# Kernel optimization log

Hardware: AMD Instinct MI355X
Metric: run time of the kernel (lower is better)

Reference implementation:

```python
import jax, jax.numpy as jnp
import numpy as np

L, S, N, E, H = 2048, 2048, 4, 1024, 16
D = E // H


def setup_inputs() -> dict:
    k0 = jax.random.key(0)
    ks = jax.random.split(k0, 11)
    std = 1.0 / np.sqrt(E)
    return {
        "query": jax.random.normal(ks[0], (L, N, E), jnp.float32),
        "key": jax.random.normal(ks[1], (S, N, E), jnp.float32),
        "value": jax.random.normal(ks[2], (S, N, E), jnp.float32),
        "Wq": jax.random.normal(ks[3], (E, E), jnp.float32) * std,
        "bq": jnp.zeros((E,), jnp.float32),
        "Wk": jax.random.normal(ks[4], (E, E), jnp.float32) * std,
        "bk": jnp.zeros((E,), jnp.float32),
        "Wv": jax.random.normal(ks[5], (E, E), jnp.float32) * std,
        "bv": jnp.zeros((E,), jnp.float32),
        "Wo": jax.random.normal(ks[6], (E, E), jnp.float32) * std,
        "bo": jnp.zeros((E,), jnp.float32),
    }


def reference(query, key, value, Wq, bq, Wk, bk, Wv, bv, Wo, bo):
    # projections (torch Linear: x @ W.T + b)
    q = query @ Wq.T + bq  # [L,N,E]
    k = key @ Wk.T + bk    # [S,N,E]
    v = value @ Wv.T + bv  # [S,N,E]
    # split heads -> [N,H,len,D]
    q = q.reshape(L, N, H, D).transpose(1, 2, 0, 3)
    k = k.reshape(S, N, H, D).transpose(1, 2, 0, 3)
    v = v.reshape(S, N, H, D).transpose(1, 2, 0, 3)
    scores = jnp.einsum("nhld,nhsd->nhls", q, k) / np.sqrt(D).astype(np.float32)
    attn_weights = jax.nn.softmax(scores, axis=-1)  # [N,H,L,S]
    out = jnp.einsum("nhls,nhsd->nhld", attn_weights, v)  # [N,H,L,D]
    out = out.transpose(2, 0, 1, 3).reshape(L, N, E)
    attn_output = out @ Wo.T + bo  # [L,N,E]
    # need_weights=True, average_attn_weights=True -> mean over heads
    return attn_output, attn_weights.mean(axis=1)
```

## Files before the change

kernel.cpp:

```cpp
#include <hip/hip_runtime.h>
#include <hip/hip_bf16.h>

typedef __attribute__((ext_vector_type(8))) short short8;
typedef __attribute__((ext_vector_type(4))) float f32x4;

#define AS1 __attribute__((address_space(1)))
#define AS3 __attribute__((address_space(3)))

__device__ __forceinline__ void gload16(const void* g, void* l) {
  __builtin_amdgcn_global_load_lds((const AS1 unsigned int*)g,
                                   (AS3 unsigned int*)l, 16, 0, 0);
}

__device__ __forceinline__ unsigned short f2bf(float x) {
  unsigned u = __float_as_uint(x);
  u = (u + 0x7FFFu + ((u >> 16) & 1u)) >> 16;
  return (unsigned short)u;
}

__device__ __forceinline__ short8 lds8(const unsigned short* p) {
  return *(const short8*)p;
}

__device__ __forceinline__ short8 lds8s(const unsigned short* base, int row, int byteInRow) {
  const int a = (row << 7) + (byteInRow ^ ((row & 7) << 4));
  return *(const short8*)((const char*)base + a);
}

#define LL 2048
#define NB 4
#define EE 1024
#define HH 16
#define DD 64
#define MROWS 8192
#define SC2 0.18033688f
#define MFIX 16.0f

__global__ __launch_bounds__(256) void conv_bf16(const float* __restrict__ src,
                                                 unsigned short* __restrict__ dst) {
  int i = blockIdx.x * 256 + threadIdx.x;
  float4 v = ((const float4*)src)[i];
  ushort4 o;
  o.x = f2bf(v.x); o.y = f2bf(v.y); o.z = f2bf(v.z); o.w = f2bf(v.w);
  ((ushort4*)dst)[i] = o;
}

template <int MODE>
__global__ __launch_bounds__(256) void gemm_bt(const unsigned short* __restrict__ A,
                                               const unsigned short* __restrict__ B,
                                               const float* __restrict__ bias,
                                               unsigned short* __restrict__ outb,
                                               float* __restrict__ outf) {
  constexpr int K = 1024;
  __shared__ __align__(16) unsigned short As[2][64 * 64];
  __shared__ __align__(16) unsigned short Bs[2][64 * 64];
  const int tid = threadIdx.x;
  const int lane = tid & 63, w = tid >> 6;
  const int wr = w >> 1, wc = w & 1;
  const int lrow = lane & 15, lg = lane >> 4;
  const int m0 = blockIdx.y * 128, n0 = blockIdx.x * 128;

  f32x4 acc[4][4] = {};

  const int sr = tid >> 3, sseg = tid & 7;
  const int slog = sseg ^ (sr & 7);
  const int mA = sr + 64 * (slog >> 2);
  const int kof = (slog & 3) * 8;
  const unsigned short* ga  = A + (size_t)(m0 + mA) * K + kof;
  const unsigned short* ga2 = A + (size_t)(m0 + mA + 32) * K + kof;
  const unsigned short* gb  = B + (size_t)(n0 + mA) * K + kof;
  const unsigned short* gb2 = B + (size_t)(n0 + mA + 32) * K + kof;

  gload16(ga,  (char*)As[0] + tid * 16);
  gload16(ga2, (char*)As[0] + tid * 16 + 4096);
  gload16(gb,  (char*)Bs[0] + tid * 16);
  gload16(gb2, (char*)Bs[0] + tid * 16 + 4096);
  __syncthreads();

  int cur = 0;
  for (int k0 = 0; k0 < K; k0 += 32) {
    if (k0 + 32 < K) {
      const int nxt = cur ^ 1;
      gload16(ga  + k0 + 32, (char*)As[nxt] + tid * 16);
      gload16(ga2 + k0 + 32, (char*)As[nxt] + tid * 16 + 4096);
      gload16(gb  + k0 + 32, (char*)Bs[nxt] + tid * 16);
      gload16(gb2 + k0 + 32, (char*)Bs[nxt] + tid * 16 + 4096);
    }

    short8 af[4], bfr[4];
#pragma unroll
    for (int mt = 0; mt < 4; ++mt)
      af[mt] = lds8s(As[cur], mt * 16 + lrow, (wr * 4 + lg) * 16);
#pragma unroll
    for (int nt = 0; nt < 4; ++nt)
      bfr[nt] = lds8s(Bs[cur], nt * 16 + lrow, (wc * 4 + lg) * 16);
#pragma unroll
    for (int mt = 0; mt < 4; ++mt)
#pragma unroll
      for (int nt = 0; nt < 4; ++nt)
        acc[mt][nt] = __builtin_amdgcn_mfma_f32_16x16x32_bf16(af[mt], bfr[nt],
                                                              acc[mt][nt], 0, 0, 0);
    __syncthreads();
    cur ^= 1;
  }

#pragma unroll
  for (int mt = 0; mt < 4; ++mt) {
#pragma unroll
    for (int nt = 0; nt < 4; ++nt) {
      const int col = n0 + wc * 64 + nt * 16 + lrow;
      const float bv = bias[col];
#pragma unroll
      for (int r = 0; r < 4; ++r) {
        const int row = m0 + wr * 64 + mt * 16 + lg * 4 + r;
        const float v = acc[mt][nt][r] + bv;
        if (MODE == 0) {
          const int l = row >> 2, n = row & 3, h = col >> 6, d = col & 63;
          outb[(((size_t)(n * HH + h)) * LL + l) * DD + d] = f2bf(v);
        } else if (MODE == 1) {
          const int s = row >> 2, n = row & 3, h = col >> 6, d = col & 63;
          outb[(((size_t)(n * HH + h)) * DD + d) * LL + s] = f2bf(v);
        } else {
          outf[(size_t)row * EE + col] = v;
        }
      }
    }
  }
}

__global__ __launch_bounds__(256) void flash_attn(const unsigned short* __restrict__ qh,
                                                  const unsigned short* __restrict__ kh,
                                                  const unsigned short* __restrict__ vth,
                                                  unsigned short* __restrict__ oh,
                                                  float* __restrict__ cT) {
  __shared__ __align__(16) unsigned short Ks[64 * 64];
  __shared__ __align__(16) unsigned short Vts[64 * 64];
  __shared__ __align__(16) unsigned short QPs[64 * 64];
  const int tid = threadIdx.x, lane = tid & 63, w = tid >> 6;
  const int lrow = lane & 15, lg = lane >> 4;
  const int nh = blockIdx.y;
  const int l0 = blockIdx.x * 64;

  const unsigned short* qbase = qh + ((size_t)nh * LL + l0) * DD;
  const unsigned short* kbase = kh + (size_t)nh * LL * DD;
  const unsigned short* vbase = vth + (size_t)nh * DD * LL;

  const int sr = tid >> 3;
  const int cs = ((tid & 7) ^ (sr & 7)) * 8;

  gload16(qbase + (size_t)sr * DD + cs,        (char*)QPs + tid * 16);
  gload16(qbase + (size_t)(sr + 32) * DD + cs, (char*)QPs + tid * 16 + 4096);
  gload16(kbase + (size_t)sr * DD + cs,        (char*)Ks + tid * 16);
  gload16(kbase + (size_t)(sr + 32) * DD + cs, (char*)Ks + tid * 16 + 4096);
  gload16(vbase + (size_t)sr * LL + cs,        (char*)Vts + tid * 16);
  gload16(vbase + (size_t)(sr + 32) * LL + cs, (char*)Vts + tid * 16 + 4096);
  __syncthreads();

  short8 qa0 = lds8s(QPs, w * 16 + lrow, lg * 16);
  short8 qa1 = lds8s(QPs, w * 16 + lrow, 64 + lg * 16);

  const short onev = (short)0x3F80;
  const short8 ones = {onev, onev, onev, onev, onev, onev, onev, onev};
  const f32x4 fz = {};

  f32x4 acco[4] = {};
  f32x4 accz = {};

  const unsigned short* kpre = kbase + (size_t)(64 + sr) * DD + cs;
  const unsigned short* vpre = vbase + (size_t)sr * LL + 64 + cs;

  const int prow = w * 16 + lrow;
#pragma unroll 1
  for (int t = 0; t < 32; ++t) {
    const bool pf = (t < 31);

    f32x4 sc[4];
    __builtin_amdgcn_s_setprio(1);
#pragma unroll
    for (int ct = 0; ct < 4; ++ct) {
      short8 b0 = lds8s(Ks, ct * 16 + lrow, lg * 16);
      short8 b1 = lds8s(Ks, ct * 16 + lrow, 64 + lg * 16);
      sc[ct] = __builtin_amdgcn_mfma_f32_16x16x32_bf16(
          b1, qa1,
          __builtin_amdgcn_mfma_f32_16x16x32_bf16(b0, qa0, fz, 0, 0, 0),
          0, 0, 0);
    }
    __builtin_amdgcn_s_setprio(0);

    __syncthreads();
    if (pf) {
      gload16(kpre,                   (char*)Ks + tid * 16);
      gload16(kpre + (size_t)32 * DD, (char*)Ks + tid * 16 + 4096);
      kpre += (size_t)64 * DD;
    }

#pragma unroll
    for (int ct = 0; ct < 4; ++ct) {
      float e0 = __builtin_exp2f(__builtin_fmaf(sc[ct][0], SC2, -MFIX));
      float e1 = __builtin_exp2f(__builtin_fmaf(sc[ct][1], SC2, -MFIX));
      float e2 = __builtin_exp2f(__builtin_fmaf(sc[ct][2], SC2, -MFIX));
      float e3 = __builtin_exp2f(__builtin_fmaf(sc[ct][3], SC2, -MFIX));
      unsigned int p0, p1;
      asm("v_cvt_pk_bf16_f32 %0, %1, %2" : "=v"(p0) : "v"(e0), "v"(e1));
      asm("v_cvt_pk_bf16_f32 %0, %1, %2" : "=v"(p1) : "v"(e2), "v"(e3));
      const int a = (prow << 7) + ((((ct * 2 + (lg >> 1)) ^ (prow & 7)) << 4) | ((lg & 1) << 3));
      uint2 u; u.x = p0; u.y = p1;
      *(uint2*)((char*)QPs + a) = u;
    }

    short8 pa0 = lds8s(QPs, prow, lg * 16);
    short8 pa1 = lds8s(QPs, prow, 64 + lg * 16);
    __builtin_amdgcn_s_setprio(1);
#pragma unroll
    for (int dt = 0; dt < 4; ++dt) {
      short8 vb0 = lds8s(Vts, dt * 16 + lrow, lg * 16);
      short8 vb1 = lds8s(Vts, dt * 16 + lrow, 64 + lg * 16);
      acco[dt] = __builtin_amdgcn_mfma_f32_16x16x32_bf16(vb0, pa0, acco[dt], 0, 0, 0);
      acco[dt] = __builtin_amdgcn_mfma_f32_16x16x32_bf16(vb1, pa1, acco[dt], 0, 0, 0);
    }
    accz = __builtin_amdgcn_mfma_f32_16x16x32_bf16(ones, pa0, accz, 0, 0, 0);
    accz = __builtin_amdgcn_mfma_f32_16x16x32_bf16(ones, pa1, accz, 0, 0, 0);
    __builtin_amdgcn_s_setprio(0);

    __syncthreads();
    if (pf) {
      gload16(vpre,                   (char*)Vts + tid * 16);
      gload16(vpre + (size_t)32 * LL, (char*)Vts + tid * 16 + 4096);
      vpre += 64;
    }
  }

  const int n = nh >> 4, h = nh & 15;
  const int lt = l0 + prow;
  const float zrow = accz[0];
  const float rz = 1.0f / zrow;
#pragma unroll
  for (int dt = 0; dt < 4; ++dt) {
    ushort4 o;
    o.x = f2bf(acco[dt][0] * rz);
    o.y = f2bf(acco[dt][1] * rz);
    o.z = f2bf(acco[dt][2] * rz);
    o.w = f2bf(acco[dt][3] * rz);
    *(ushort4*)&oh[((size_t)lt * NB + n) * EE + h * 64 + dt * 16 + lg * 4] = o;
  }
  if (lg == 0) {
    cT[((size_t)n * LL + lt) * HH + h] = -(MFIX + __builtin_log2f(zrow));
  }
}

__global__ __launch_bounds__(256) void weights_mean(const unsigned short* __restrict__ qh,
                                                    const unsigned short* __restrict__ kh,
                                                    const float* __restrict__ cT,
                                                    float* __restrict__ out1) {
  __shared__ __align__(16) unsigned short Qs[64 * 64];
  __shared__ __align__(16) unsigned short Ks[64 * 64];
  const int tid = threadIdx.x, lane = tid & 63, w = tid >> 6;
  const int lrow = lane & 15, lg = lane >> 4;
  const int n = blockIdx.z;
  const int l0 = blockIdx.y * 64, s0 = blockIdx.x * 64;

  const int sr = tid >> 3;
  const int cs = ((tid & 7) ^ (sr & 7)) * 8;
  const f32x4 fz = {};

  float accw[4][4] = {};
  for (int h = 0; h < HH; ++h) {
    const int nh = n * HH + h;
    __syncthreads();
    const unsigned short* qbase = qh + ((size_t)nh * LL + l0) * DD;
    const unsigned short* kbase = kh + ((size_t)nh * LL + s0) * DD;
    gload16(qbase + (size_t)sr * DD + cs,        (char*)Qs + tid * 16);
    gload16(qbase + (size_t)(sr + 32) * DD + cs, (char*)Qs + tid * 16 + 4096);
    gload16(kbase + (size_t)sr * DD + cs,        (char*)Ks + tid * 16);
    gload16(kbase + (size_t)(sr + 32) * DD + cs, (char*)Ks + tid * 16 + 4096);
    __syncthreads();

    short8 qa0 = lds8s(Qs, w * 16 + lrow, lg * 16);
    short8 qa1 = lds8s(Qs, w * 16 + lrow, 64 + lg * 16);
    f32x4 sc[4];
    __builtin_amdgcn_s_setprio(1);
#pragma unroll
    for (int ct = 0; ct < 4; ++ct) {
      short8 b0 = lds8s(Ks, ct * 16 + lrow, lg * 16);
      short8 b1 = lds8s(Ks, ct * 16 + lrow, 64 + lg * 16);
      sc[ct] = __builtin_amdgcn_mfma_f32_16x16x32_bf16(
          qa1, b1,
          __builtin_amdgcn_mfma_f32_16x16x32_bf16(qa0, b0, fz, 0, 0, 0),
          0, 0, 0);
    }
    __builtin_amdgcn_s_setprio(0);
#pragma unroll
    for (int r = 0; r < 4; ++r) {
      const int lt = l0 + w * 16 + lg * 4 + r;
      const float c = cT[((size_t)n * LL + lt) * HH + h];
#pragma unroll
      for (int ct = 0; ct < 4; ++ct)
        accw[ct][r] += __builtin_exp2f(__builtin_fmaf(sc[ct][r], SC2, c));
    }
  }
#pragma unroll
  for (int ct = 0; ct < 4; ++ct)
#pragma unroll
    for (int r = 0; r < 4; ++r) {
      const int lt = l0 + w * 16 + lg * 4 + r;
      const int s = s0 + ct * 16 + lrow;
      out1[((size_t)n * LL + lt) * LL + s] = accw[ct][r] * 0.0625f;
    }
}

extern "C" void kernel_launch(void* const* d_in, const int* in_sizes, int n_in,
                              void* d_out, int out_size, void* d_ws, size_t ws_size,
                              hipStream_t stream) {
  const float* query = (const float*)d_in[0];
  const float* key   = (const float*)d_in[1];
  const float* value = (const float*)d_in[2];
  const float* Wq = (const float*)d_in[3];
  const float* bq = (const float*)d_in[4];
  const float* Wk = (const float*)d_in[5];
  const float* bk = (const float*)d_in[6];
  const float* Wv = (const float*)d_in[7];
  const float* bv = (const float*)d_in[8];
  const float* Wo = (const float*)d_in[9];
  const float* bo = (const float*)d_in[10];

  float* out0 = (float*)d_out;
  float* out1 = out0 + (size_t)LL * NB * EE;

  char* ws = (char*)d_ws;
  unsigned short* xbuf = (unsigned short*)(ws + 0);
  unsigned short* wqb  = (unsigned short*)(ws + 16777216);
  unsigned short* wkb  = (unsigned short*)(ws + 18874368);
  unsigned short* wvb  = (unsigned short*)(ws + 20971520);
  unsigned short* wob  = (unsigned short*)(ws + 23068672);
  unsigned short* qhb  = (unsigned short*)(ws + 25165824);
  unsigned short* khb  = (unsigned short*)(ws + 41943040);
  unsigned short* vthb = (unsigned short*)(ws + 58720256);
  float* cT   = (float*)(ws + 75497472);

  const int nTok = MROWS * EE;
  const int nW   = EE * EE;

  conv_bf16<<<nW / 1024, 256, 0, stream>>>(Wq, wqb);
  conv_bf16<<<nW / 1024, 256, 0, stream>>>(Wk, wkb);
  conv_bf16<<<nW / 1024, 256, 0, stream>>>(Wv, wvb);
  conv_bf16<<<nW / 1024, 256, 0, stream>>>(Wo, wob);

  dim3 ggrid(EE / 128, MROWS / 128);

  conv_bf16<<<nTok / 1024, 256, 0, stream>>>(query, xbuf);
  gemm_bt<0><<<ggrid, 256, 0, stream>>>(xbuf, wqb, bq, qhb, nullptr);
  conv_bf16<<<nTok / 1024, 256, 0, stream>>>(key, xbuf);
  gemm_bt<0><<<ggrid, 256, 0, stream>>>(xbuf, wkb, bk, khb, nullptr);
  conv_bf16<<<nTok / 1024, 256, 0, stream>>>(value, xbuf);
  gemm_bt<1><<<ggrid, 256, 0, stream>>>(xbuf, wvb, bv, vthb, nullptr);

  flash_attn<<<dim3(LL / 64, NB * HH), 256, 0, stream>>>(qhb, khb, vthb, xbuf, cT);

  gemm_bt<2><<<ggrid, 256, 0, stream>>>(xbuf, wob, bo, nullptr, out0);

  weights_mean<<<dim3(LL / 64, LL / 64, NB), 256, 0, stream>>>(qhb, khb, cT, out1);
}
```

Before: 388.0 us.

## Process 128 query rows per flash-attention block to reuse K/V tiles

Each flash-attention block now handles 128 query rows, with each wave owning two 16-row subtiles, instead of 64 rows. Every K and V tile loaded into LDS is used by twice as many rows, halving global K/V traffic and barrier count per row. The softmax exp of the first subtile is placed between the two score MFMA groups to overlap ALU with matrix work. The cost is more registers and LDS per block and half as many blocks in the grid, which reduces occupancy and parallel slack.

```diff
diff --git a/kernel.cpp b/kernel.cpp
--- a/kernel.cpp
+++ b/kernel.cpp
@@ -135,11 +135,11 @@
                                                   float* __restrict__ cT) {
   __shared__ __align__(16) unsigned short Ks[64 * 64];
   __shared__ __align__(16) unsigned short Vts[64 * 64];
-  __shared__ __align__(16) unsigned short QPs[64 * 64];
+  __shared__ __align__(16) unsigned short QPs[128 * 64];
   const int tid = threadIdx.x, lane = tid & 63, w = tid >> 6;
   const int lrow = lane & 15, lg = lane >> 4;
   const int nh = blockIdx.y;
-  const int l0 = blockIdx.x * 64;
+  const int l0 = blockIdx.x * 128;
 
   const unsigned short* qbase = qh + ((size_t)nh * LL + l0) * DD;
   const unsigned short* kbase = kh + (size_t)nh * LL * DD;
@@ -148,41 +148,74 @@
   const int sr = tid >> 3;
   const int cs = ((tid & 7) ^ (sr & 7)) * 8;
 
-  gload16(qbase + (size_t)sr * DD + cs,        (char*)QPs + tid * 16);
-  gload16(qbase + (size_t)(sr + 32) * DD + cs, (char*)QPs + tid * 16 + 4096);
+#pragma unroll
+  for (int c = 0; c < 4; ++c)
+    gload16(qbase + (size_t)(c * 32 + sr) * DD + cs, (char*)QPs + c * 4096 + tid * 16);
   gload16(kbase + (size_t)sr * DD + cs,        (char*)Ks + tid * 16);
   gload16(kbase + (size_t)(sr + 32) * DD + cs, (char*)Ks + tid * 16 + 4096);
   gload16(vbase + (size_t)sr * LL + cs,        (char*)Vts + tid * 16);
   gload16(vbase + (size_t)(sr + 32) * LL + cs, (char*)Vts + tid * 16 + 4096);
   __syncthreads();
 
-  short8 qa0 = lds8s(QPs, w * 16 + lrow, lg * 16);
-  short8 qa1 = lds8s(QPs, w * 16 + lrow, 64 + lg * 16);
+  short8 qa[2][2];
+#pragma unroll
+  for (int qs = 0; qs < 2; ++qs) {
+    qa[qs][0] = lds8s(QPs, w * 32 + qs * 16 + lrow, lg * 16);
+    qa[qs][1] = lds8s(QPs, w * 32 + qs * 16 + lrow, 64 + lg * 16);
+  }
 
   const short onev = (short)0x3F80;
   const short8 ones = {onev, onev, onev, onev, onev, onev, onev, onev};
   const f32x4 fz = {};
 
-  f32x4 acco[4] = {};
-  f32x4 accz = {};
+  f32x4 acco[2][4] = {};
+  f32x4 accz[2] = {};
 
   const unsigned short* kpre = kbase + (size_t)(64 + sr) * DD + cs;
   const unsigned short* vpre = vbase + (size_t)sr * LL + 64 + cs;
 
-  const int prow = w * 16 + lrow;
+  const int prow0 = w * 32 + lrow;
+
 #pragma unroll 1
   for (int t = 0; t < 32; ++t) {
     const bool pf = (t < 31);
 
-    f32x4 sc[4];
+    f32x4 sc0[4];
     __builtin_amdgcn_s_setprio(1);
 #pragma unroll
     for (int ct = 0; ct < 4; ++ct) {
       short8 b0 = lds8s(Ks, ct * 16 + lrow, lg * 16);
       short8 b1 = lds8s(Ks, ct * 16 + lrow, 64 + lg * 16);
-      sc[ct] = __builtin_amdgcn_mfma_f32_16x16x32_bf16(
-          b1, qa1,
-          __builtin_amdgcn_mfma_f32_16x16x32_bf16(b0, qa0, fz, 0, 0, 0),
+      sc0[ct] = __builtin_amdgcn_mfma_f32_16x16x32_bf16(
+          b1, qa[0][1],
+          __builtin_amdgcn_mfma_f32_16x16x32_bf16(b0, qa[0][0], fz, 0, 0, 0),
+          0, 0, 0);
+    }
+    __builtin_amdgcn_s_setprio(0);
+
+#pragma unroll
+    for (int ct = 0; ct < 4; ++ct) {
+      float e0 = __builtin_exp2f(__builtin_fmaf(sc0[ct][0], SC2, -MFIX));
+      float e1 = __builtin_exp2f(__builtin_fmaf(sc0[ct][1], SC2, -MFIX));
+      float e2 = __builtin_exp2f(__builtin_fmaf(sc0[ct][2], SC2, -MFIX));
+      float e3 = __builtin_exp2f(__builtin_fmaf(sc0[ct][3], SC2, -MFIX));
+      unsigned int p0, p1;
+      asm("v_cvt_pk_bf16_f32 %0, %1, %2" : "=v"(p0) : "v"(e0), "v"(e1));
+      asm("v_cvt_pk_bf16_f32 %0, %1, %2" : "=v"(p1) : "v"(e2), "v"(e3));
+      const int a = (prow0 << 7) + ((((ct * 2 + (lg >> 1)) ^ (prow0 & 7)) << 4) | ((lg & 1) << 3));
+      uint2 u; u.x = p0; u.y = p1;
+      *(uint2*)((char*)QPs + a) = u;
+    }
+
+    f32x4 sc1[4];
+    __builtin_amdgcn_s_setprio(1);
+#pragma unroll
+    for (int ct = 0; ct < 4; ++ct) {
+      short8 b0 = lds8s(Ks, ct * 16 + lrow, lg * 16);
+      short8 b1 = lds8s(Ks, ct * 16 + lrow, 64 + lg * 16);
+      sc1[ct] = __builtin_amdgcn_mfma_f32_16x16x32_bf16(
+          b1, qa[1][1],
+          __builtin_amdgcn_mfma_f32_16x16x32_bf16(b0, qa[1][0], fz, 0, 0, 0),
           0, 0, 0);
     }
     __builtin_amdgcn_s_setprio(0);
@@ -194,32 +227,39 @@
       kpre += (size_t)64 * DD;
     }
 
+    const int prow1 = prow0 + 16;
 #pragma unroll
     for (int ct = 0; ct < 4; ++ct) {
-      float e0 = __builtin_exp2f(__builtin_fmaf(sc[ct][0], SC2, -MFIX));
-      float e1 = __builtin_exp2f(__builtin_fmaf(sc[ct][1], SC2, -MFIX));
-      float e2 = __builtin_exp2f(__builtin_fmaf(sc[ct][2], SC2, -MFIX));
-      float e3 = __builtin_exp2f(__builtin_fmaf(sc[ct][3], SC2, -MFIX));
+      float e0 = __builtin_exp2f(__builtin_fmaf(sc1[ct][0], SC2, -MFIX));
+      float e1 = __builtin_exp2f(__builtin_fmaf(sc1[ct][1], SC2, -MFIX));
+      float e2 = __builtin_exp2f(__builtin_fmaf(sc1[ct][2], SC2, -MFIX));
+      float e3 = __builtin_exp2f(__builtin_fmaf(sc1[ct][3], SC2, -MFIX));
       unsigned int p0, p1;
       asm("v_cvt_pk_bf16_f32 %0, %1, %2" : "=v"(p0) : "v"(e0), "v"(e1));
       asm("v_cvt_pk_bf16_f32 %0, %1, %2" : "=v"(p1) : "v"(e2), "v"(e3));
-      const int a = (prow << 7) + ((((ct * 2 + (lg >> 1)) ^ (prow & 7)) << 4) | ((lg & 1) << 3));
+      const int a = (prow1 << 7) + ((((ct * 2 + (lg >> 1)) ^ (prow1 & 7)) << 4) | ((lg & 1) << 3));
       uint2 u; u.x = p0; u.y = p1;
       *(uint2*)((char*)QPs + a) = u;
     }
 
-    short8 pa0 = lds8s(QPs, prow, lg * 16);
-    short8 pa1 = lds8s(QPs, prow, 64 + lg * 16);
+    short8 pa00 = lds8s(QPs, prow0, lg * 16);
+    short8 pa01 = lds8s(QPs, prow0, 64 + lg * 16);
+    short8 pa10 = lds8s(QPs, prow1, lg * 16);
+    short8 pa11 = lds8s(QPs, prow1, 64 + lg * 16);
     __builtin_amdgcn_s_setprio(1);
 #pragma unroll
     for (int dt = 0; dt < 4; ++dt) {
       short8 vb0 = lds8s(Vts, dt * 16 + lrow, lg * 16);
       short8 vb1 = lds8s(Vts, dt * 16 + lrow, 64 + lg * 16);
-      acco[dt] = __builtin_amdgcn_mfma_f32_16x16x32_bf16(vb0, pa0, acco[dt], 0, 0, 0);
-      acco[dt] = __builtin_amdgcn_mfma_f32_16x16x32_bf16(vb1, pa1, acco[dt], 0, 0, 0);
-    }
-    accz = __builtin_amdgcn_mfma_f32_16x16x32_bf16(ones, pa0, accz, 0, 0, 0);
-    accz = __builtin_amdgcn_mfma_f32_16x16x32_bf16(ones, pa1, accz, 0, 0, 0);
+      acco[0][dt] = __builtin_amdgcn_mfma_f32_16x16x32_bf16(vb0, pa00, acco[0][dt], 0, 0, 0);
+      acco[0][dt] = __builtin_amdgcn_mfma_f32_16x16x32_bf16(vb1, pa01, acco[0][dt], 0, 0, 0);
+      acco[1][dt] = __builtin_amdgcn_mfma_f32_16x16x32_bf16(vb0, pa10, acco[1][dt], 0, 0, 0);
+      acco[1][dt] = __builtin_amdgcn_mfma_f32_16x16x32_bf16(vb1, pa11, acco[1][dt], 0, 0, 0);
+    }
+    accz[0] = __builtin_amdgcn_mfma_f32_16x16x32_bf16(ones, pa00, accz[0], 0, 0, 0);
+    accz[0] = __builtin_amdgcn_mfma_f32_16x16x32_bf16(ones, pa01, accz[0], 0, 0, 0);
+    accz[1] = __builtin_amdgcn_mfma_f32_16x16x32_bf16(ones, pa10, accz[1], 0, 0, 0);
+    accz[1] = __builtin_amdgcn_mfma_f32_16x16x32_bf16(ones, pa11, accz[1], 0, 0, 0);
     __builtin_amdgcn_s_setprio(0);
 
     __syncthreads();
@@ -231,20 +271,23 @@
   }
 
   const int n = nh >> 4, h = nh & 15;
-  const int lt = l0 + prow;
-  const float zrow = accz[0];
-  const float rz = 1.0f / zrow;
-#pragma unroll
-  for (int dt = 0; dt < 4; ++dt) {
-    ushort4 o;
-    o.x = f2bf(acco[dt][0] * rz);
-    o.y = f2bf(acco[dt][1] * rz);
-    o.z = f2bf(acco[dt][2] * rz);
-    o.w = f2bf(acco[dt][3] * rz);
-    *(ushort4*)&oh[((size_t)lt * NB + n) * EE + h * 64 + dt * 16 + lg * 4] = o;
-  }
-  if (lg == 0) {
-    cT[((size_t)n * LL + lt) * HH + h] = -(MFIX + __builtin_log2f(zrow));
+#pragma unroll
+  for (int qs = 0; qs < 2; ++qs) {
+    const int lt = l0 + w * 32 + qs * 16 + lrow;
+    const float zrow = accz[qs][0];
+    const float rz = 1.0f / zrow;
+#pragma unroll
+    for (int dt = 0; dt < 4; ++dt) {
+      ushort4 o;
+      o.x = f2bf(acco[qs][dt][0] * rz);
+      o.y = f2bf(acco[qs][dt][1] * rz);
+      o.z = f2bf(acco[qs][dt][2] * rz);
+      o.w = f2bf(acco[qs][dt][3] * rz);
+      *(ushort4*)&oh[((size_t)lt * NB + n) * EE + h * 64 + dt * 16 + lg * 4] = o;
+    }
+    if (lg == 0) {
+      cT[((size_t)n * LL + lt) * HH + h] = -(MFIX + __builtin_log2f(zrow));
+    }
   }
 }
 
@@ -354,7 +397,7 @@
   conv_bf16<<<nTok / 1024, 256, 0, stream>>>(value, xbuf);
   gemm_bt<1><<<ggrid, 256, 0, stream>>>(xbuf, wvb, bv, vthb, nullptr);
 
-  flash_attn<<<dim3(LL / 64, NB * HH), 256, 0, stream>>>(qhb, khb, vthb, xbuf, cT);
+  flash_attn<<<dim3(LL / 128, NB * HH), 256, 0, stream>>>(qhb, khb, vthb, xbuf, cT);
 
   gemm_bt<2><<<ggrid, 256, 0, stream>>>(xbuf, wob, bo, nullptr, out0);
 
```

Result: faster. 378.5 us (-2.5%).
